# Optimization experiments

Measured on AMD Instinct MI355X. Metric: run time of the kernel, lower is better.

Reference implementation:

```python
import math
import jax, jax.numpy as jnp
import numpy as np

VMIN, VMAX, NUM_BINS = 0.0, 1.0, 64
BIN_WIDTH = (VMAX - VMIN) / NUM_BINS
SIGMA = BIN_WIDTH * (1.0 / (2.0 * math.sqrt(2.0 * math.log(2.0))))
EPS = 1e-10


def setup_inputs() -> dict:
    key = jax.random.key(0)
    kx, ky = jax.random.split(key)
    shape = (2, 1, 96, 96, 96)
    x = jax.random.uniform(kx, shape, dtype=jnp.float32)
    y = jax.random.uniform(ky, shape, dtype=jnp.float32)
    return {"x": x, "y": y}


def _gauss_win(v, bins):
    # v: (N, P), bins: (B,) -> (N, B, P)
    d = v[:, None, :] - bins[None, :, None]
    # NOTE: faithful to source: exp(.)/sqrt(2*pi) * sigma (multiplies by sigma)
    return jnp.exp(-(d * d) / (2.0 * SIGMA * SIGMA)) / math.sqrt(2.0 * math.pi) * SIGMA


def reference(x, y):
    N = x.shape[0]
    xf = x.reshape(N, -1)  # (N, P); dim=1 channel folded into P
    yf = y.reshape(N, -1)
    bins = jnp.linspace(VMIN, VMAX, NUM_BINS, dtype=x.dtype)
    win_x = _gauss_win(xf, bins)  # (N, B, P)
    win_y = _gauss_win(yf, bins)  # (N, B, P)
    hist_joint = jnp.einsum('nbp,ncp->nbc', win_x, win_y)  # (N, B, B)
    hist_norm = hist_joint.sum(axis=(1, 2)) + EPS
    p_joint = hist_joint / hist_norm[:, None, None]
    p_x = p_joint.sum(axis=2)
    p_y = p_joint.sum(axis=1)
    ent_x = -jnp.sum(p_x * jnp.log(p_x + EPS), axis=1)
    ent_y = -jnp.sum(p_y * jnp.log(p_y + EPS), axis=1)
    ent_joint = -jnp.sum(p_joint * jnp.log(p_joint + EPS), axis=(1, 2))
    # normalised=True branch
    return -jnp.mean((ent_x + ent_y) / ent_joint)
```

## Files before the change

### kernel.cpp

```cpp
#include <hip/hip_runtime.h>
#include <math.h>


#define NBINS 64
#define BK 240
#define LDA (BK + 8)
#define NKB (BK / 16)

typedef _Float16 half8   __attribute__((ext_vector_type(8)));
typedef float    floatx16 __attribute__((ext_vector_type(16)));

static constexpr double kSigmaD = 0.015625 / 2.3548200450309493;
static constexpr double kAcD    = (1.0 / (63.0 * 63.0)) / (2.0 * kSigmaD * kSigmaD);
static constexpr float  kAc     = (float)kAcD;
static constexpr float  kEps    = 1e-10f;

__global__ void zero_ws_kernel(float* __restrict__ hist, float* __restrict__ out, int n) {
    int i = blockIdx.x * blockDim.x + threadIdx.x;
    if (i < n) hist[i] = 0.0f;
    if (i == 0) out[0] = 0.0f;
}

__global__ __launch_bounds__(256) void hist_gemm_kernel(
        const float* __restrict__ x, const float* __restrict__ y,
        float* __restrict__ hist, int P, int elemsPerBlock) {
    __shared__ _Float16 Ax[NBINS * LDA];
    __shared__ _Float16 By[NBINS * LDA];

    const int t    = threadIdx.x;
    const int lane = t & 63;
    const int wave = t >> 6;
    const int qi   = wave >> 1;
    const int qj   = wave & 1;
    const int n    = blockIdx.y;

    {
        float* a4 = (float*)Ax;
        float* b4 = (float*)By;
        const int ndw = NBINS * LDA / 2;
        for (int i = t; i < ndw; i += 256) { a4[i] = 0.0f; b4[i] = 0.0f; }
    }

    floatx16 acc = {};
    const float* __restrict__ xp = x + (size_t)n * P;
    const float* __restrict__ yp = y + (size_t)n * P;
    const int base    = blockIdx.x * elemsPerBlock;
    const int nElems  = elemsPerBlock;
    const int nChunks = (nElems + BK - 1) / BK;

    int pcx = 2, pcy = 2;
    __syncthreads();

    for (int c = 0; c < nChunks; ++c) {
        const int off = c * BK + t;
        float wx[5], wy[5];
        int cx = 2, cy = 2;
        const bool valid = (t < BK) && (off < nElems);
        if (valid) {
            const float vx = xp[base + off] * 63.0f;
            const float vy = yp[base + off] * 63.0f;
            cx = min(max((int)(vx + 0.5f), 2), 61);
            cy = min(max((int)(vy + 0.5f), 2), 61);
            const float dx = vx - (float)cx;
            const float dy = vy - (float)cy;
#pragma unroll
            for (int k = 0; k < 5; ++k) {
                const float ddx = dx - (float)(k - 2);
                const float ddy = dy - (float)(k - 2);
                wx[k] = __expf(-kAc * ddx * ddx);
                wy[k] = __expf(-kAc * ddy * ddy);
            }
        } else {
#pragma unroll
            for (int k = 0; k < 5; ++k) { wx[k] = 0.0f; wy[k] = 0.0f; }
        }

        if (t < BK) {
#pragma unroll
            for (int k = 0; k < 5; ++k) {
                Ax[(pcx - 2 + k) * LDA + t] = (_Float16)0.0f;
                By[(pcy - 2 + k) * LDA + t] = (_Float16)0.0f;
            }
#pragma unroll
            for (int k = 0; k < 5; ++k) {
                Ax[(cx - 2 + k) * LDA + t] = (_Float16)wx[k];
                By[(cy - 2 + k) * LDA + t] = (_Float16)wy[k];
            }
        }
        pcx = cx; pcy = cy;
        __syncthreads();

        const int rA = qi * 32 + (lane & 31);
        const int rB = qj * 32 + (lane & 31);
        const int kq = 8 * (lane >> 5);
#pragma unroll
        for (int kb = 0; kb < NKB; ++kb) {
            const half8 a = *(const half8*)&Ax[rA * LDA + kb * 16 + kq];
            const half8 b = *(const half8*)&By[rB * LDA + kb * 16 + kq];
            acc = __builtin_amdgcn_mfma_f32_32x32x16_f16(a, b, acc, 0, 0, 0);
        }
        __syncthreads();
    }

    float* __restrict__ gh = hist + (size_t)n * NBINS * NBINS;
#pragma unroll
    for (int r = 0; r < 16; ++r) {
        const int row = qi * 32 + (r & 3) + 8 * (r >> 2) + 4 * (lane >> 5);
        const int col = qj * 32 + (lane & 31);
        atomicAdd(&gh[row * NBINS + col], acc[r]);
    }
}

__device__ __forceinline__ float block_sum_bcast(float v, float* sm) {
#pragma unroll
    for (int off = 32; off > 0; off >>= 1) v += __shfl_down(v, off, 64);
    __syncthreads();
    const int lane = threadIdx.x & 63;
    const int wid  = threadIdx.x >> 6;
    if (lane == 0) sm[wid] = v;
    __syncthreads();
    return sm[0] + sm[1] + sm[2] + sm[3];
}

__global__ __launch_bounds__(256) void finalize_kernel(
        const float* __restrict__ hist, float* __restrict__ out) {
    __shared__ float sm[4];
    __shared__ float sx[NBINS];
    __shared__ float sy[NBINS];

    const int n = blockIdx.x;
    const float* __restrict__ h = hist + (size_t)n * NBINS * NBINS;

    float s = 0.0f;
    for (int i = threadIdx.x; i < NBINS * NBINS; i += 256) s += h[i];
    const float S = block_sum_bcast(s, sm) + kEps;
    const float invS = 1.0f / S;

    float ej = 0.0f;
    for (int i = threadIdx.x; i < NBINS * NBINS; i += 256) {
        const float p = h[i] * invS;
        ej += p * __logf(p + kEps);
    }

    if (threadIdx.x < NBINS) {
        float px = 0.0f;
        const float* rp = &h[threadIdx.x * NBINS];
        for (int c = 0; c < NBINS; c++) px += rp[c];
        px *= invS;
        sx[threadIdx.x] = px * __logf(px + kEps);
    } else if (threadIdx.x < 2 * NBINS) {
        const int c = threadIdx.x - NBINS;
        float py = 0.0f;
        for (int b = 0; b < NBINS; b++) py += h[b * NBINS + c];
        py *= invS;
        sy[c] = py * __logf(py + kEps);
    }

    const float EJ = block_sum_bcast(ej, sm);
    const float mx = (threadIdx.x < NBINS) ? sx[threadIdx.x] : 0.0f;
    const float my = (threadIdx.x < NBINS) ? sy[threadIdx.x] : 0.0f;
    const float EX = block_sum_bcast(mx, sm);
    const float EY = block_sum_bcast(my, sm);

    if (threadIdx.x == 0) atomicAdd(out, -0.5f * ((EX + EY) / EJ));
}

extern "C" void kernel_launch(void* const* d_in, const int* in_sizes, int n_in,
                              void* d_out, int out_size, void* d_ws, size_t ws_size,
                              hipStream_t stream) {
    const float* x = (const float*)d_in[0];
    const float* y = (const float*)d_in[1];
    float* hist = (float*)d_ws;
    float* out  = (float*)d_out;

    const int N = 2;
    const int P = in_sizes[0] / N;
    const int blocksPerN = 256;
    const int elemsPerBlock = P / blocksPerN;

    const int histElems = N * NBINS * NBINS;
    zero_ws_kernel<<<(histElems + 255) / 256, 256, 0, stream>>>(hist, out, histElems);

    dim3 grid(blocksPerN, N);
    hist_gemm_kernel<<<grid, 256, 0, stream>>>(x, y, hist, P, elemsPerBlock);

    finalize_kernel<<<2, 256, 0, stream>>>(hist, out);
}
```

Before: 101.5 us.

## Split MFMA K-dimension across waves, prefetch next chunk, reduce partials in LDS

Each wave now computes the full 64x64 output over a quarter of the K blocks, with four accumulators, instead of one 32x32 quadrant over all K. The four per-wave partials are reduced through shared memory before the global atomics. Next-chunk loads and the Gaussian weight computation are moved after the MFMAs to overlap with them, and the zeroing kernel becomes hipMemsetAsync. This adds more accumulator registers and an LDS reduction, in exchange for fewer redundant LDS fragment loads and overlapped global loads.

Result: slower. 107.8 us (+6.3%).

```diff
diff --git a/kernel.cpp b/kernel.cpp
--- a/kernel.cpp
+++ b/kernel.cpp
@@ -4,10 +4,10 @@
 
 #define NBINS 64
 #define BK 240
-#define LDA (BK + 8)
-#define NKB (BK / 16)
-
-typedef _Float16 half8   __attribute__((ext_vector_type(8)));
+#define LDA 248
+#define NKB 15
+
+typedef _Float16 half8    __attribute__((ext_vector_type(8)));
 typedef float    floatx16 __attribute__((ext_vector_type(16)));
 
 static constexpr double kSigmaD = 0.015625 / 2.3548200450309493;
@@ -15,66 +15,70 @@
 static constexpr float  kAc     = (float)kAcD;
 static constexpr float  kEps    = 1e-10f;
 
-__global__ void zero_ws_kernel(float* __restrict__ hist, float* __restrict__ out, int n) {
-    int i = blockIdx.x * blockDim.x + threadIdx.x;
-    if (i < n) hist[i] = 0.0f;
-    if (i == 0) out[0] = 0.0f;
+__device__ __forceinline__ void make_weights(float vx, float vy, bool valid,
+                                             int& cx, int& cy,
+                                             float* wx, float* wy) {
+    cx = 2; cy = 2;
+#pragma unroll
+    for (int k = 0; k < 5; ++k) { wx[k] = 0.0f; wy[k] = 0.0f; }
+    if (valid) {
+        cx = min(max((int)(vx + 0.5f), 2), 61);
+        cy = min(max((int)(vy + 0.5f), 2), 61);
+        const float dx = vx - (float)cx;
+        const float dy = vy - (float)cy;
+#pragma unroll
+        for (int k = 0; k < 5; ++k) {
+            const float ddx = dx - (float)(k - 2);
+            const float ddy = dy - (float)(k - 2);
+            wx[k] = __expf(-kAc * ddx * ddx);
+            wy[k] = __expf(-kAc * ddy * ddy);
+        }
+    }
 }
 
 __global__ __launch_bounds__(256) void hist_gemm_kernel(
         const float* __restrict__ x, const float* __restrict__ y,
         float* __restrict__ hist, int P, int elemsPerBlock) {
-    __shared__ _Float16 Ax[NBINS * LDA];
-    __shared__ _Float16 By[NBINS * LDA];
+    __shared__ __align__(16) _Float16 tiles[2 * NBINS * LDA];
+    _Float16* Ax = tiles;
+    _Float16* By = tiles + NBINS * LDA;
 
     const int t    = threadIdx.x;
     const int lane = t & 63;
     const int wave = t >> 6;
-    const int qi   = wave >> 1;
-    const int qj   = wave & 1;
+    const int m    = lane & 31;
+    const int kq   = 8 * (lane >> 5);
     const int n    = blockIdx.y;
 
     {
-        float* a4 = (float*)Ax;
-        float* b4 = (float*)By;
-        const int ndw = NBINS * LDA / 2;
-        for (int i = t; i < ndw; i += 256) { a4[i] = 0.0f; b4[i] = 0.0f; }
-    }
-
-    floatx16 acc = {};
+        float* z4 = (float*)tiles;
+        const int ndw = 2 * NBINS * LDA / 2;
+        for (int i = t; i < ndw; i += 256) z4[i] = 0.0f;
+    }
+
+    floatx16 acc[2][2];
+#pragma unroll
+    for (int bi = 0; bi < 2; ++bi)
+#pragma unroll
+        for (int bj = 0; bj < 2; ++bj) acc[bi][bj] = (floatx16){};
+
     const float* __restrict__ xp = x + (size_t)n * P;
     const float* __restrict__ yp = y + (size_t)n * P;
     const int base    = blockIdx.x * elemsPerBlock;
     const int nElems  = elemsPerBlock;
     const int nChunks = (nElems + BK - 1) / BK;
 
+    int cx, cy; float wx[5], wy[5];
+    {
+        const bool valid = (t < BK) && (t < nElems);
+        float vx = 0.0f, vy = 0.0f;
+        if (valid) { vx = xp[base + t] * 63.0f; vy = yp[base + t] * 63.0f; }
+        make_weights(vx, vy, valid, cx, cy, wx, wy);
+    }
     int pcx = 2, pcy = 2;
     __syncthreads();
 
     for (int c = 0; c < nChunks; ++c) {
-        const int off = c * BK + t;
-        float wx[5], wy[5];
-        int cx = 2, cy = 2;
-        const bool valid = (t < BK) && (off < nElems);
-        if (valid) {
-            const float vx = xp[base + off] * 63.0f;
-            const float vy = yp[base + off] * 63.0f;
-            cx = min(max((int)(vx + 0.5f), 2), 61);
-            cy = min(max((int)(vy + 0.5f), 2), 61);
-            const float dx = vx - (float)cx;
-            const float dy = vy - (float)cy;
-#pragma unroll
-            for (int k = 0; k < 5; ++k) {
-                const float ddx = dx - (float)(k - 2);
-                const float ddy = dy - (float)(k - 2);
-                wx[k] = __expf(-kAc * ddx * ddx);
-                wy[k] = __expf(-kAc * ddy * ddy);
-            }
-        } else {
-#pragma unroll
-            for (int k = 0; k < 5; ++k) { wx[k] = 0.0f; wy[k] = 0.0f; }
-        }
-
         if (t < BK) {
 #pragma unroll
             for (int k = 0; k < 5; ++k) {
@@ -90,25 +94,67 @@
         pcx = cx; pcy = cy;
         __syncthreads();
 
-        const int rA = qi * 32 + (lane & 31);
-        const int rB = qj * 32 + (lane & 31);
-        const int kq = 8 * (lane >> 5);
-#pragma unroll
-        for (int kb = 0; kb < NKB; ++kb) {
-            const half8 a = *(const half8*)&Ax[rA * LDA + kb * 16 + kq];
-            const half8 b = *(const half8*)&By[rB * LDA + kb * 16 + kq];
-            acc = __builtin_amdgcn_mfma_f32_32x32x16_f16(a, b, acc, 0, 0, 0);
-        }
+        float vx = 0.0f, vy = 0.0f; bool valid = false;
+        if (c + 1 < nChunks) {
+            const int off = (c + 1) * BK + t;
+            valid = (t < BK) && (off < nElems);
+            if (valid) { vx = xp[base + off] * 63.0f; vy = yp[base + off] * 63.0f; }
+        }
+
+#pragma unroll
+        for (int s = 0; s < 4; ++s) {
+            const int kb = wave + 4 * s;
+            if (kb >= NKB) break;
+            const int ko = kb * 16 + kq;
+            const half8 a0 = *(const half8*)&Ax[m * LDA + ko];
+            const half8 a1 = *(const half8*)&Ax[(32 + m) * LDA + ko];
+            const half8 b0 = *(const half8*)&By[m * LDA + ko];
+            const half8 b1 = *(const half8*)&By[(32 + m) * LDA + ko];
+            acc[0][0] = __builtin_amdgcn_mfma_f32_32x32x16_f16(a0, b0, acc[0][0], 0, 0, 0);
+            acc[0][1] = __builtin_amdgcn_mfma_f32_32x32x16_f16(a0, b1, acc[0][1], 0, 0, 0);
+            acc[1][0] = __builtin_amdgcn_mfma_f32_32x32x16_f16(a1, b0, acc[1][0], 0, 0, 0);
+            acc[1][1] = __builtin_amdgcn_mfma_f32_32x32x16_f16(a1, b1, acc[1][1], 0, 0, 0);
+        }
+
+        make_weights(vx, vy, valid, cx, cy, wx, wy);
         __syncthreads();
     }
 
+    float* cred = (float*)tiles;
+    const int rbase = 4 * (lane >> 5);
+
+    if (wave >= 2) {
+        const int off = (wave - 2) * 4096;
+#pragma unroll
+        for (int bi = 0; bi < 2; ++bi)
+#pragma unroll
+            for (int bj = 0; bj < 2; ++bj)
+#pragma unroll
+                for (int r = 0; r < 16; ++r) {
+                    const int row = bi * 32 + (r & 3) + 8 * (r >> 2) + rbase;
+                    const int col = bj * 32 + m;
+                    cred[off + row * NBINS + col] = acc[bi][bj][r];
+                }
+    }
+    __syncthreads();
+    if (wave < 2) {
+        const int off = wave * 4096;
+#pragma unroll
+        for (int bi = 0; bi < 2; ++bi)
+#pragma unroll
+            for (int bj = 0; bj < 2; ++bj)
+#pragma unroll
+                for (int r = 0; r < 16; ++r) {
+                    const int row = bi * 32 + (r & 3) + 8 * (r >> 2) + rbase;
+                    const int col = bj * 32 + m;
+                    const int idx = off + row * NBINS + col;
+                    cred[idx] = acc[bi][bj][r] + cred[idx];
+                }
+    }
+    __syncthreads();
     float* __restrict__ gh = hist + (size_t)n * NBINS * NBINS;
-#pragma unroll
-    for (int r = 0; r < 16; ++r) {
-        const int row = qi * 32 + (r & 3) + 8 * (r >> 2) + 4 * (lane >> 5);
-        const int col = qj * 32 + (lane & 31);
-        atomicAdd(&gh[row * NBINS + col], acc[r]);
-    }
+    for (int i = t; i < NBINS * NBINS; i += 256)
+        atomicAdd(&gh[i], cred[i] + cred[4096 + i]);
 }
 
 __device__ __forceinline__ float block_sum_bcast(float v, float* sm) {
@@ -178,8 +224,8 @@
     const int blocksPerN = 256;
     const int elemsPerBlock = P / blocksPerN;
 
-    const int histElems = N * NBINS * NBINS;
-    zero_ws_kernel<<<(histElems + 255) / 256, 256, 0, stream>>>(hist, out, histElems);
+    hipMemsetAsync(hist, 0, (size_t)N * NBINS * NBINS * sizeof(float), stream);
+    hipMemsetAsync(out, 0, sizeof(float), stream);
 
     dim3 grid(blocksPerN, N);
     hist_gemm_kernel<<<grid, 256, 0, stream>>>(x, y, hist, P, elemsPerBlock);
```
